# Optimization experiments

Hardware: AMD Instinct MI355X
Metric: run time of the kernel (lower is better)

Reference implementation:

```python
import jax, jax.numpy as jnp
import numpy as np
import math

VOCAB = 32000
D = 2048
H = 16
KVH = 4
HD = D // H          # 128
FF = 5632
L = 2
S = 2048
B = 1
EPS = 1e-5
ROPE_BASE = 10000.0


def setup_inputs() -> dict:
    key = jax.random.key(0)
    ks = jax.random.split(key, 12)
    sc = 0.02
    # RoPE table: [S, HD//2, 2] (cos, sin), matching precompute_freqs_cis
    inv = 1.0 / (ROPE_BASE ** (jnp.arange(0, HD, 2, dtype=jnp.float32) / HD))
    pos = jnp.arange(S, dtype=jnp.float32)
    f = jnp.outer(pos, inv)
    freqs_cis = jnp.stack([jnp.cos(f), jnp.sin(f)], axis=-1)
    mask = jnp.tril(jnp.ones((S, S), dtype=bool))
    return {
        "input_ids": jax.random.randint(ks[0], (B, S), 0, VOCAB, dtype=jnp.int32),
        "mask": mask,
        "freqs_cis": freqs_cis,
        "w_embed": jax.random.normal(ks[1], (VOCAB, D), jnp.float32) * sc,
        "wqkv": jax.random.normal(ks[2], (L, D, D + 2 * KVH * HD), jnp.float32) * sc,
        "wo": jax.random.normal(ks[3], (L, D, D), jnp.float32) * sc,
        "w1": jax.random.normal(ks[4], (L, D, FF), jnp.float32) * sc,
        "w3": jax.random.normal(ks[5], (L, D, FF), jnp.float32) * sc,
        "w2": jax.random.normal(ks[6], (L, FF, D), jnp.float32) * sc,
        "attn_norm_w": jnp.ones((L, D), jnp.float32),
        "ff_norm_w": jnp.ones((L, D), jnp.float32),
        "final_norm_w": jnp.ones((D,), jnp.float32),
        "w_head": jax.random.normal(ks[7], (D, VOCAB), jnp.float32) * sc,
    }


def _rmsnorm(x, w):
    xf = x.astype(jnp.float32)
    n = xf * jax.lax.rsqrt(jnp.mean(xf * xf, axis=-1, keepdims=True) + EPS)
    return n.astype(x.dtype) * w


def _rope(x, fc):
    # x: [b, h, s, hd]; fc: [s, hd/2, 2]
    xr = x.reshape(*x.shape[:-1], HD // 2, 2)
    cos, sin = fc[..., 0], fc[..., 1]  # [s, hd/2] broadcast over b,h
    out = jnp.stack([xr[..., 0] * cos - xr[..., 1] * sin,
                     xr[..., 1] * cos + xr[..., 0] * sin], axis=-1)
    return out.reshape(x.shape).astype(x.dtype)


def _attention(x, mask, fc, wqkv, wo):
    b, s, _ = x.shape
    qkv = x @ wqkv  # [b, s, D + 2*kv_dim]
    kv_dim = KVH * HD
    q, k, v = jnp.split(qkv, [D, D + kv_dim], axis=-1)
    q = q.reshape(b, s, H, HD).transpose(0, 2, 1, 3)      # [b,H,s,hd]
    k = k.reshape(b, s, KVH, HD).transpose(0, 2, 1, 3)    # [b,KVH,s,hd]
    v = v.reshape(b, s, KVH, HD).transpose(0, 2, 1, 3)
    q = _rope(q, fc)
    k = _rope(k, fc)
    rep = H // KVH
    k = jnp.repeat(k, rep, axis=1)  # [b,H,s,hd]
    v = jnp.repeat(v, rep, axis=1)
    scores = jnp.einsum('bhqd,bhkd->bhqk', q, k) / math.sqrt(HD)
    scores = jnp.where(mask, scores, -1e30)
    attn = jax.nn.softmax(scores, axis=-1)
    out = jnp.einsum('bhqk,bhkd->bhqd', attn, v)
    out = out.transpose(0, 2, 1, 3).reshape(b, s, D)
    return out @ wo


def reference(input_ids, mask, freqs_cis, w_embed, wqkv, wo, w1, w3, w2,
              attn_norm_w, ff_norm_w, final_norm_w, w_head):
    x = w_embed[input_ids]  # [B,S,D]
    for l in range(L):
        h = x + _attention(_rmsnorm(x, attn_norm_w[l]), mask, freqs_cis,
                           wqkv[l], wo[l])
        hn = _rmsnorm(h, ff_norm_w[l])
        x = h + (jax.nn.silu(hn @ w1[l]) * (hn @ w3[l])) @ w2[l]
    x = _rmsnorm(x, final_norm_w)
    return x @ w_head  # [B,S,VOCAB]
```

## Files before the change

kernel.cpp:

```cpp
#include <hip/hip_runtime.h>

#define DD 2048
#define SEQ 2048
#define NH 16
#define NKV 4
#define HD 128
#define FFD 5632
#define NL 2

typedef __bf16 bf16x8 __attribute__((ext_vector_type(8)));
typedef float f32x4 __attribute__((ext_vector_type(4)));

__device__ __forceinline__ unsigned short f2bf(float f) {
    unsigned int u = __builtin_bit_cast(unsigned int, f);
    u += 0x7fffu + ((u >> 16) & 1u);
    return (unsigned short)(u >> 16);
}

__global__ __launch_bounds__(256)
void embed_gather(const int* __restrict__ ids, const float* __restrict__ wemb,
                  float* __restrict__ x)
{
    int s = blockIdx.x;
    int id = ids[s];
    const float4* src = (const float4*)(wemb + (size_t)id * DD);
    float4* dst = (float4*)(x + (size_t)s * DD);
    dst[threadIdx.x] = src[threadIdx.x];
    dst[threadIdx.x + 256] = src[threadIdx.x + 256];
}

__global__ __launch_bounds__(256)
void rmsnorm_bf16(const float* __restrict__ x, const float* __restrict__ w,
                  unsigned short* __restrict__ out)
{
    int row = blockIdx.x;
    int t = threadIdx.x;
    const float4* xr = (const float4*)(x + (size_t)row * DD);
    float4 v0 = xr[t], v1 = xr[t + 256];
    float ss = v0.x * v0.x + v0.y * v0.y + v0.z * v0.z + v0.w * v0.w
             + v1.x * v1.x + v1.y * v1.y + v1.z * v1.z + v1.w * v1.w;
#pragma unroll
    for (int off = 32; off; off >>= 1) ss += __shfl_down(ss, off);
    __shared__ float red[4];
    if ((t & 63) == 0) red[t >> 6] = ss;
    __syncthreads();
    float sc = rsqrtf((red[0] + red[1] + red[2] + red[3]) * (1.0f / DD) + 1e-5f);
    const float4* wr = (const float4*)w;
    float4 w0 = wr[t], w1v = wr[t + 256];
    ushort4 o0, o1;
    o0.x = f2bf(v0.x * sc * w0.x);  o0.y = f2bf(v0.y * sc * w0.y);
    o0.z = f2bf(v0.z * sc * w0.z);  o0.w = f2bf(v0.w * sc * w0.w);
    o1.x = f2bf(v1.x * sc * w1v.x); o1.y = f2bf(v1.y * sc * w1v.y);
    o1.z = f2bf(v1.z * sc * w1v.z); o1.w = f2bf(v1.w * sc * w1v.w);
    ushort4* op = (ushort4*)(out + (size_t)row * DD);
    op[t] = o0;
    op[t + 256] = o1;
}

__global__ __launch_bounds__(256)
void transpose_cast(const float* __restrict__ src, unsigned short* __restrict__ dst,
                    int ld_src, int ld_dst, size_t sb, size_t db)
{
    __shared__ float tile[64][65];
    src += (size_t)blockIdx.z * sb;
    dst += (size_t)blockIdx.z * db;
    int c0 = blockIdx.x * 64, r0 = blockIdx.y * 64;
    int tx = threadIdx.x & 15, ty = threadIdx.x >> 4;
#pragma unroll
    for (int i = 0; i < 4; ++i) {
        int r = ty + i * 16;
        float4 v = *(const float4*)(src + (size_t)(r0 + r) * ld_src + c0 + tx * 4);
        tile[r][tx * 4 + 0] = v.x; tile[r][tx * 4 + 1] = v.y;
        tile[r][tx * 4 + 2] = v.z; tile[r][tx * 4 + 3] = v.w;
    }
    __syncthreads();
#pragma unroll
    for (int i = 0; i < 4; ++i) {
        int c = ty + i * 16;
        ushort4 o;
        o.x = f2bf(tile[tx * 4 + 0][c]); o.y = f2bf(tile[tx * 4 + 1][c]);
        o.z = f2bf(tile[tx * 4 + 2][c]); o.w = f2bf(tile[tx * 4 + 3][c]);
        *(ushort4*)(dst + (size_t)(c0 + c) * ld_dst + r0 + tx * 4) = o;
    }
}

__global__ void rope_qk(const float* __restrict__ qkv, const float* __restrict__ fc,
                        unsigned short* __restrict__ Qb, unsigned short* __restrict__ Kb)
{
    int s = blockIdx.x;
    int hh = blockIdx.y;
    int i = threadIdx.x;
    float2 cs = *(const float2*)(fc + ((size_t)s * 64 + i) * 2);
    const float* src;
    unsigned short* dst;
    if (hh < NH) {
        src = qkv + (size_t)s * 3072 + hh * HD;
        dst = Qb + ((size_t)hh * SEQ + s) * HD;
    } else {
        int kh = hh - NH;
        src = qkv + (size_t)s * 3072 + DD + kh * HD;
        dst = Kb + ((size_t)kh * SEQ + s) * HD;
    }
    float2 xv = *(const float2*)(src + 2 * i);
    ushort2 o;
    o.x = f2bf(xv.x * cs.x - xv.y * cs.y);
    o.y = f2bf(xv.y * cs.x + xv.x * cs.y);
    *(ushort2*)(dst + 2 * i) = o;
}

__global__ __launch_bounds__(256)
void silu_mul(const float* __restrict__ h, unsigned short* __restrict__ g)
{
    size_t i = (size_t)blockIdx.x * 256 + threadIdx.x;
    size_t row = i / (FFD / 4), c4 = i % (FFD / 4);
    const float* p = h + row * (2 * FFD) + c4 * 4;
    float4 a = *(const float4*)(p);
    float4 b = *(const float4*)(p + FFD);
    ushort4 o;
    o.x = f2bf(a.x / (1.f + __expf(-a.x)) * b.x);
    o.y = f2bf(a.y / (1.f + __expf(-a.y)) * b.y);
    o.z = f2bf(a.z / (1.f + __expf(-a.z)) * b.z);
    o.w = f2bf(a.w / (1.f + __expf(-a.w)) * b.w);
    *(ushort4*)(g + row * FFD + c4 * 4) = o;
}

__global__ __launch_bounds__(256)
void gemm_bf16(const unsigned short* __restrict__ A, const unsigned short* __restrict__ B,
               float* __restrict__ C, const float* __restrict__ Res,
               int N, int K, int mT)
{
    __shared__ __attribute__((aligned(16))) unsigned char smem[65536];
    const int tid = threadIdx.x;
    const int lane = tid & 63;
    const int w = tid >> 6;
    const int nwg = gridDim.x;
    const int qq = nwg >> 3;
    const int logical = ((int)blockIdx.x & 7) * qq + ((int)blockIdx.x >> 3);
    const int m0 = (logical % mT) * 128;
    const int n0 = (logical / mT) * 128;
    const int wm = (w >> 1) * 64, wn = (w & 1) * 64;
    const int lrow = lane & 15, lgrp = lane >> 4;
    const int NT = K >> 6;

    f32x4 acc[4][4];
#pragma unroll
    for (int i = 0; i < 4; ++i)
#pragma unroll
        for (int j = 0; j < 4; ++j) acc[i][j] = 0.f;

    auto stage = [&](int bsel, int kt) {
#pragma unroll
        for (int it = 0; it < 4; ++it) {
            int o = it * 4096 + tid * 16;
            int row = o >> 7;
            int col = (o & 127) ^ ((row & 7) << 4);
            const char* ga = (const char*)A + ((size_t)(m0 + row) * K + kt) * 2 + col;
            const char* gb = (const char*)B + ((size_t)(n0 + row) * K + kt) * 2 + col;
            __builtin_amdgcn_global_load_lds(
                (__attribute__((address_space(1))) const void*)ga,
                (__attribute__((address_space(3))) void*)(smem + bsel * 32768 + it * 4096 + w * 1024),
                16, 0, 0);
            __builtin_amdgcn_global_load_lds(
                (__attribute__((address_space(1))) const void*)gb,
                (__attribute__((address_space(3))) void*)(smem + bsel * 32768 + 16384 + it * 4096 + w * 1024),
                16, 0, 0);
        }
    };

    stage(0, 0);
    int cur = 0;
    for (int t = 0; t < NT; ++t) {
        if (t + 1 < NT) {
            stage(cur ^ 1, (t + 1) << 6);
            asm volatile("s_waitcnt vmcnt(8)" ::: "memory");
        } else {
            asm volatile("s_waitcnt vmcnt(0)" ::: "memory");
        }
        __builtin_amdgcn_s_barrier();
        __builtin_amdgcn_sched_barrier(0);
        const unsigned char* buf = smem + cur * 32768;
#pragma unroll
        for (int kk = 0; kk < 2; ++kk) {
            bf16x8 af[4], bfr[4];
            int cb = kk * 64 + lgrp * 16;
#pragma unroll
            for (int i = 0; i < 4; ++i) {
                int ra = wm + i * 16 + lrow;
                af[i] = *(const bf16x8*)(buf + ra * 128 + (cb ^ ((ra & 7) << 4)));
                int rb = wn + i * 16 + lrow;
                bfr[i] = *(const bf16x8*)(buf + 16384 + rb * 128 + (cb ^ ((rb & 7) << 4)));
            }
#pragma unroll
            for (int i = 0; i < 4; ++i)
#pragma unroll
                for (int j = 0; j < 4; ++j)
                    acc[i][j] = __builtin_amdgcn_mfma_f32_16x16x32_bf16(af[i], bfr[j], acc[i][j], 0, 0, 0);
        }
        __builtin_amdgcn_s_barrier();
        cur ^= 1;
    }

    const bool hasRes = (Res != nullptr);
#pragma unroll
    for (int i = 0; i < 4; ++i)
#pragma unroll
        for (int j = 0; j < 4; ++j) {
            int r = m0 + wm + i * 16 + lgrp * 4;
            int c = n0 + wn + j * 16 + lrow;
#pragma unroll
            for (int jj = 0; jj < 4; ++jj) {
                size_t idx = (size_t)(r + jj) * N + c;
                float v = acc[i][j][jj];
                if (hasRes) v += Res[idx];
                C[idx] = v;
            }
        }
}

__global__ __launch_bounds__(256)
void attn_fwd(const unsigned short* __restrict__ Qb, const unsigned short* __restrict__ Kb,
              const unsigned short* __restrict__ VTb, unsigned short* __restrict__ O)
{
    __shared__ __attribute__((aligned(16))) unsigned char smem[40960];
    const int qb = 31 - (int)blockIdx.x;
    const int h = blockIdx.y;
    const int kvh = h >> 2;
    const int tid = threadIdx.x, lane = tid & 63, w = tid >> 6;
    const int lrow = lane & 15, lgrp = lane >> 4;
    const int q0 = qb * 64 + w * 16;

    bf16x8 qf[4];
    const unsigned short* qrow = Qb + ((size_t)h * SEQ + q0 + lrow) * HD;
#pragma unroll
    for (int c = 0; c < 4; ++c)
        qf[c] = *(const bf16x8*)(qrow + c * 32 + lgrp * 8);

    float m[4], l[4];
    f32x4 oacc[8];
#pragma unroll
    for (int j = 0; j < 8; ++j) oacc[j] = 0.f;
#pragma unroll
    for (int j = 0; j < 4; ++j) { m[j] = -3.0e38f; l[j] = 0.f; }

    const float scale = 0.08838834764831845f;
    const char* kbase = (const char*)(Kb + (size_t)kvh * SEQ * HD);
    const char* vbase = (const char*)(VTb + (size_t)kvh * HD * SEQ);
    unsigned char* Pl = smem + 32768 + w * 2048;

    for (int t = 0; t <= qb; ++t) {
        __syncthreads();
#pragma unroll
        for (int it = 0; it < 4; ++it) {
            int o = it * 4096 + tid * 16;
            int row = o >> 8, col = o & 255;
            bf16x8 kv = *(const bf16x8*)(kbase + (size_t)(t * 64 + row) * 256 + col);
            *(bf16x8*)(smem + (o ^ ((row & 7) << 4))) = kv;
            int row2 = o >> 7, col2 = o & 127;
            bf16x8 vv = *(const bf16x8*)(vbase + (size_t)row2 * (SEQ * 2) + (size_t)t * 128 + col2);
            *(bf16x8*)(smem + 16384 + (o ^ ((row2 & 7) << 4))) = vv;
        }
        __syncthreads();

        f32x4 sf[4];
#pragma unroll
        for (int kf = 0; kf < 4; ++kf) sf[kf] = 0.f;
#pragma unroll
        for (int kf = 0; kf < 4; ++kf) {
            int rb = kf * 16 + lrow;
            int rbase = rb * 256;
            int sw = (rb & 7) << 4;
#pragma unroll
            for (int c = 0; c < 4; ++c) {
                bf16x8 kfr = *(const bf16x8*)(smem + rbase + ((c * 64 + lgrp * 16) ^ sw));
                sf[kf] = __builtin_amdgcn_mfma_f32_16x16x32_bf16(qf[c], kfr, sf[kf], 0, 0, 0);
            }
        }
        const bool diag = (t == qb);
        float mx[4] = {-3.0e38f, -3.0e38f, -3.0e38f, -3.0e38f};
#pragma unroll
        for (int kf = 0; kf < 4; ++kf)
#pragma unroll
            for (int j = 0; j < 4; ++j) {
                float v = sf[kf][j] * scale;
                if (diag && (t * 64 + kf * 16 + lrow) > (q0 + lgrp * 4 + j)) v = -3.0e38f;
                sf[kf][j] = v;
                mx[j] = fmaxf(mx[j], v);
            }
#pragma unroll
        for (int off = 1; off < 16; off <<= 1)
#pragma unroll
            for (int j = 0; j < 4; ++j) mx[j] = fmaxf(mx[j], __shfl_xor(mx[j], off));
        float alpha[4], rs[4];
#pragma unroll
        for (int j = 0; j < 4; ++j) {
            float mn = fmaxf(m[j], mx[j]);
            alpha[j] = __expf(m[j] - mn);
            m[j] = mn;
            rs[j] = 0.f;
        }
#pragma unroll
        for (int kf = 0; kf < 4; ++kf)
#pragma unroll
            for (int j = 0; j < 4; ++j) {
                float p = __expf(sf[kf][j] - m[j]);
                rs[j] += p;
                int qq = lgrp * 4 + j;
                int addr = qq * 128 + (((kf * 16 + lrow) * 2) ^ ((qq & 7) << 4));
                *(unsigned short*)(Pl + addr) = f2bf(p);
            }
#pragma unroll
        for (int off = 1; off < 16; off <<= 1)
#pragma unroll
            for (int j = 0; j < 4; ++j) rs[j] += __shfl_xor(rs[j], off);
#pragma unroll
        for (int j = 0; j < 4; ++j) l[j] = l[j] * alpha[j] + rs[j];
#pragma unroll
        for (int hf = 0; hf < 8; ++hf)
#pragma unroll
            for (int j = 0; j < 4; ++j) oacc[hf][j] *= alpha[j];
#pragma unroll
        for (int c = 0; c < 2; ++c) {
            int cb = c * 64 + lgrp * 16;
            bf16x8 pf = *(const bf16x8*)(Pl + lrow * 128 + (cb ^ ((lrow & 7) << 4)));
#pragma unroll
            for (int hf = 0; hf < 8; ++hf) {
                int rv = hf * 16 + lrow;
                bf16x8 vf = *(const bf16x8*)(smem + 16384 + rv * 128 + (cb ^ ((rv & 7) << 4)));
                oacc[hf] = __builtin_amdgcn_mfma_f32_16x16x32_bf16(pf, vf, oacc[hf], 0, 0, 0);
            }
        }
    }
#pragma unroll
    for (int hf = 0; hf < 8; ++hf)
#pragma unroll
        for (int j = 0; j < 4; ++j) {
            float v = oacc[hf][j] / l[j];
            int qg = q0 + lgrp * 4 + j;
            O[(size_t)qg * DD + h * HD + hf * 16 + lrow] = f2bf(v);
        }
}

extern "C" void kernel_launch(void* const* d_in, const int* in_sizes, int n_in,
                              void* d_out, int out_size, void* d_ws, size_t ws_size,
                              hipStream_t stream)
{
    (void)in_sizes; (void)n_in; (void)out_size; (void)ws_size;
    const int* ids = (const int*)d_in[0];
    const float* fc   = (const float*)d_in[2];
    const float* wemb = (const float*)d_in[3];
    const float* wqkv = (const float*)d_in[4];
    const float* wo   = (const float*)d_in[5];
    const float* w1   = (const float*)d_in[6];
    const float* w3   = (const float*)d_in[7];
    const float* w2   = (const float*)d_in[8];
    const float* anw  = (const float*)d_in[9];
    const float* fnw  = (const float*)d_in[10];
    const float* finw = (const float*)d_in[11];
    const float* wh   = (const float*)d_in[12];
    float* out = (float*)d_out;
    char* ws = (char*)d_ws;

    unsigned short* WQKVT = (unsigned short*)(ws);
    unsigned short* WOT   = (unsigned short*)(ws + 25165824);
    unsigned short* W13T  = (unsigned short*)(ws + 41943040);
    unsigned short* W2T   = (unsigned short*)(ws + 134217728);
    unsigned short* WHT   = (unsigned short*)(ws + 180355072);
    float*          X     = (float*)(ws + 311427072);
    unsigned short* XN    = (unsigned short*)(ws + 328204288);
    float*          QKV   = (float*)(ws + 336592896);
    unsigned short* Qb    = (unsigned short*)(ws + 361758720);
    unsigned short* Kb    = (unsigned short*)(ws + 370147328);
    unsigned short* VT    = (unsigned short*)(ws + 372244480);
    unsigned short* AO    = (unsigned short*)(ws + 374341632);
    float*          H13   = (float*)(ws + 382730240);
    unsigned short* G     = (unsigned short*)(ws + 475004928);

    transpose_cast<<<dim3(48, 32, 2), 256, 0, stream>>>(wqkv, WQKVT, 3072, 2048,
        (size_t)2048 * 3072, (size_t)3072 * 2048);
    transpose_cast<<<dim3(32, 32, 2), 256, 0, stream>>>(wo, WOT, 2048, 2048,
        (size_t)2048 * 2048, (size_t)2048 * 2048);
    transpose_cast<<<dim3(88, 32, 2), 256, 0, stream>>>(w1, W13T, 5632, 2048,
        (size_t)2048 * 5632, (size_t)11264 * 2048);
    transpose_cast<<<dim3(88, 32, 2), 256, 0, stream>>>(w3, W13T + (size_t)5632 * 2048, 5632, 2048,
        (size_t)2048 * 5632, (size_t)11264 * 2048);
    transpose_cast<<<dim3(32, 88, 2), 256, 0, stream>>>(w2, W2T, 2048, 5632,
        (size_t)5632 * 2048, (size_t)2048 * 5632);
    transpose_cast<<<dim3(500, 32, 1), 256, 0, stream>>>(wh, WHT, 32000, 2048, 0, 0);

    embed_gather<<<dim3(SEQ), 256, 0, stream>>>(ids, wemb, X);

    for (int lyr = 0; lyr < NL; ++lyr) {
        const unsigned short* wqkvT_l = WQKVT + (size_t)lyr * 3072 * 2048;
        const unsigned short* woT_l   = WOT   + (size_t)lyr * 2048 * 2048;
        const unsigned short* w13T_l  = W13T  + (size_t)lyr * 11264 * 2048;
        const unsigned short* w2T_l   = W2T   + (size_t)lyr * 2048 * 5632;

        rmsnorm_bf16<<<dim3(SEQ), 256, 0, stream>>>(X, anw + lyr * DD, XN);
        gemm_bf16<<<dim3(24 * 16), 256, 0, stream>>>(XN, wqkvT_l, QKV, nullptr, 3072, 2048, 16);
        rope_qk<<<dim3(SEQ, NH + NKV), 64, 0, stream>>>(QKV, fc, Qb, Kb);
        transpose_cast<<<dim3(2, 32, 4), 256, 0, stream>>>(QKV + 2560, VT, 3072, 2048,
            128, (size_t)128 * 2048);
        attn_fwd<<<dim3(32, NH), 256, 0, stream>>>(Qb, Kb, VT, AO);
        gemm_bf16<<<dim3(16 * 16), 256, 0, stream>>>(AO, woT_l, X, X, 2048, 2048, 16);
        rmsnorm_bf16<<<dim3(SEQ), 256, 0, stream>>>(X, fnw + lyr * DD, XN);
        gemm_bf16<<<dim3(88 * 16), 256, 0, stream>>>(XN, w13T_l, H13, nullptr, 11264, 2048, 16);
        silu_mul<<<dim3(11264), 256, 0, stream>>>(H13, G);
        gemm_bf16<<<dim3(16 * 16), 256, 0, stream>>>(G, w2T_l, X, X, 2048, 5632, 16);
    }
    rmsnorm_bf16<<<dim3(SEQ), 256, 0, stream>>>(X, finw, XN);
    gemm_bf16<<<dim3(250 * 16), 256, 0, stream>>>(XN, WHT, out, nullptr, 32000, 2048, 16);
}
```

Measured before the change: 1.316 ms.

## Add 256x256-tile GEMM with direct-to-LDS loads for FFN-up and LM head

Adds a new 512-thread GEMM kernel that uses 256x256 output tiles, double-buffered LDS filled via global_load_lds, XOR-swizzled LDS layout, an XCD-aware block remap and setprio around the MFMA bursts. It replaces the 128-tile GEMM for the two largest GEMMs (w1/w3 projection and vocab head). The larger tile raises arithmetic intensity and cuts global traffic per FLOP. In exchange it uses 128KB LDS and one block per CU, which lowers occupancy and tail efficiency on the smaller grids.

```diff
diff --git a/kernel.cpp b/kernel.cpp
--- a/kernel.cpp
+++ b/kernel.cpp
@@ -217,6 +217,114 @@
         }
 }
 
+__global__ __launch_bounds__(512, 1)
+void gemm_bf16_256(const unsigned short* __restrict__ A, const unsigned short* __restrict__ B,
+                   float* __restrict__ C, int N, int K, int mT)
+{
+    __shared__ __attribute__((aligned(16))) unsigned char smem[131072];
+    const int tid = threadIdx.x;
+    const int lane = tid & 63;
+    const int w = tid >> 6;
+    const int nwg = gridDim.x;
+    const int qq = nwg >> 3;
+    const int logical = ((int)blockIdx.x & 7) * qq + ((int)blockIdx.x >> 3);
+    const int m0 = (logical % mT) * 256;
+    const int n0 = (logical / mT) * 256;
+    const int wm2 = (w >> 2) * 128;
+    const int wn4 = (w & 3) * 64;
+    const int lrow = lane & 15, lgrp = lane >> 4;
+    const int NT = K >> 6;
+
+    f32x4 acc[8][4];
+#pragma unroll
+    for (int i = 0; i < 8; ++i)
+#pragma unroll
+        for (int j = 0; j < 4; ++j) acc[i][j] = 0.f;
+
+    auto stage = [&](int bsel, int kt, int pair) {
+        int o = pair * 8192 + tid * 16;
+        int row = o >> 7;
+        int col = (o & 127) ^ ((row & 7) << 4);
+        const char* ga = (const char*)A + ((size_t)(m0 + row) * K + kt) * 2 + col;
+        const char* gb = (const char*)B + ((size_t)(n0 + row) * K + kt) * 2 + col;
+        __builtin_amdgcn_global_load_lds(
+            (__attribute__((address_space(1))) const void*)ga,
+            (__attribute__((address_space(3))) void*)(smem + bsel * 65536 + pair * 8192 + w * 1024),
+            16, 0, 0);
+        __builtin_amdgcn_global_load_lds(
+            (__attribute__((address_space(1))) const void*)gb,
+            (__attribute__((address_space(3))) void*)(smem + bsel * 65536 + 32768 + pair * 8192 + w * 1024),
+            16, 0, 0);
+    };
+
+#pragma unroll
+    for (int p = 0; p < 4; ++p) stage(0, 0, p);
+
+    int cur = 0;
+    for (int t = 0; t < NT; ++t) {
+        const bool havenext = (t + 1 < NT);
+        const int ktn = (t + 1) << 6;
+        const unsigned char* buf = smem + cur * 65536;
+        bf16x8 bfr[4][2];
+#pragma unroll
+        for (int p = 0; p < 4; ++p) {
+            if (p == 0) {
+                if (havenext) {
+                    stage(cur ^ 1, ktn, 0);
+                    asm volatile("s_waitcnt vmcnt(2)" ::: "memory");
+                } else {
+                    asm volatile("s_waitcnt vmcnt(0)" ::: "memory");
+                }
+                __builtin_amdgcn_s_barrier();
+                __builtin_amdgcn_sched_barrier(0);
+#pragma unroll
+                for (int nj = 0; nj < 4; ++nj)
+#pragma unroll
+                    for (int kk = 0; kk < 2; ++kk) {
+                        int rb = wn4 + nj * 16 + lrow;
+                        int cb = kk * 64 + lgrp * 16;
+                        bfr[nj][kk] = *(const bf16x8*)(buf + 32768 + rb * 128 + (cb ^ ((rb & 7) << 4)));
+                    }
+            } else {
+                if (havenext) stage(cur ^ 1, ktn, p);
+                __builtin_amdgcn_s_barrier();
+            }
+            bf16x8 afr[2][2];
+#pragma unroll
+            for (int i = 0; i < 2; ++i)
+#pragma unroll
+                for (int kk = 0; kk < 2; ++kk) {
+                    int ra = wm2 + (p * 2 + i) * 16 + lrow;
+                    int cb = kk * 64 + lgrp * 16;
+                    afr[i][kk] = *(const bf16x8*)(buf + ra * 128 + (cb ^ ((ra & 7) << 4)));
+                }
+            __builtin_amdgcn_s_setprio(1);
+#pragma unroll
+            for (int i = 0; i < 2; ++i)
+#pragma unroll
+                for (int nj = 0; nj < 4; ++nj)
+#pragma unroll
+                    for (int kk = 0; kk < 2; ++kk)
+                        acc[p * 2 + i][nj] = __builtin_amdgcn_mfma_f32_16x16x32_bf16(
+                            afr[i][kk], bfr[nj][kk], acc[p * 2 + i][nj], 0, 0, 0);
+            __builtin_amdgcn_s_setprio(0);
+        }
+        __builtin_amdgcn_s_barrier();
+        cur ^= 1;
+    }
+
+#pragma unroll
+    for (int mi = 0; mi < 8; ++mi)
+#pragma unroll
+        for (int nj = 0; nj < 4; ++nj) {
+            int r = m0 + wm2 + mi * 16 + lgrp * 4;
+            int c = n0 + wn4 + nj * 16 + lrow;
+#pragma unroll
+            for (int jj = 0; jj < 4; ++jj)
+                C[(size_t)(r + jj) * N + c] = acc[mi][nj][jj];
+        }
+}
+
 __global__ __launch_bounds__(256)
 void attn_fwd(const unsigned short* __restrict__ Qb, const unsigned short* __restrict__ Kb,
               const unsigned short* __restrict__ VTb, unsigned short* __restrict__ O)
@@ -403,10 +511,10 @@
         attn_fwd<<<dim3(32, NH), 256, 0, stream>>>(Qb, Kb, VT, AO);
         gemm_bf16<<<dim3(16 * 16), 256, 0, stream>>>(AO, woT_l, X, X, 2048, 2048, 16);
         rmsnorm_bf16<<<dim3(SEQ), 256, 0, stream>>>(X, fnw + lyr * DD, XN);
-        gemm_bf16<<<dim3(88 * 16), 256, 0, stream>>>(XN, w13T_l, H13, nullptr, 11264, 2048, 16);
+        gemm_bf16_256<<<dim3(8 * 44), 512, 0, stream>>>(XN, w13T_l, H13, 11264, 2048, 8);
         silu_mul<<<dim3(11264), 256, 0, stream>>>(H13, G);
         gemm_bf16<<<dim3(16 * 16), 256, 0, stream>>>(G, w2T_l, X, X, 2048, 5632, 16);
     }
     rmsnorm_bf16<<<dim3(SEQ), 256, 0, stream>>>(X, finw, XN);
-    gemm_bf16<<<dim3(250 * 16), 256, 0, stream>>>(XN, WHT, out, nullptr, 32000, 2048, 16);
-}
+    gemm_bf16_256<<<dim3(8 * 125), 512, 0, stream>>>(XN, WHT, out, 32000, 2048, 8);
+}
```

After: 1.315 ms. No clear change (-0.1%).
